# Performance work log

Hardware: AMD Instinct MI355X
Metric: run time of the kernel (lower is better)

## Reference

```python
import jax, jax.numpy as jnp
import numpy as np
import math
from jax import lax

# Fixed Poincare-ball curvature (hypll Curvature() initializes to 1.0; treated as constant here).
C_CURV = 1.0
EPS = 1e-15

def _beta(a, b):
    # Euler Beta function via lgamma (Python-level constant, computed at trace time).
    return math.exp(math.lgamma(a) + math.lgamma(b) - math.lgamma(a + b))

def logmap0(x, axis):
    # log map at the origin of the Poincare ball along `axis` (the manifold dim).
    sc = jnp.sqrt(C_CURV)
    n = jnp.sqrt(jnp.clip(jnp.sum(x * x, axis=axis, keepdims=True), EPS))
    return jnp.arctanh(jnp.clip(sc * n, 0.0, 1.0 - 1e-7)) * x / (sc * n)

def expmap0(v, axis):
    sc = jnp.sqrt(C_CURV)
    n = jnp.sqrt(jnp.clip(jnp.sum(v * v, axis=axis, keepdims=True), EPS))
    return jnp.tanh(sc * n) * v / (sc * n)

def poincare_fc(x, z, r):
    # HNN++ Poincare fully-connected layer (as in hypll): unidirectional MLR -> sinh -> ball projection.
    # x: (..., Nin) ball points, z: (Nin, Nout), r: (Nout,)
    rc = jnp.sqrt(C_CURV)
    z_norm = jnp.sqrt(jnp.clip(jnp.sum(z * z, axis=0), EPS))  # (Nout,)
    z_unit = z / z_norm
    drcr = 2.0 * rc * r
    rcx = rc * x
    cx2 = jnp.sum(rcx * rcx, axis=-1, keepdims=True)
    num = 2.0 * (rcx @ z_unit) * jnp.cosh(drcr) - (1.0 + cx2) * jnp.sinh(drcr)
    mlr = (2.0 * z_norm / rc) * jnp.arcsinh(num / jnp.clip(1.0 - cx2, EPS))
    y = jnp.sinh(rc * mlr) / rc
    return y / (1.0 + jnp.sqrt(1.0 + C_CURV * jnp.sum(y * y, axis=-1, keepdims=True)))

def hconv2d(x, z, r, k, pad):
    # Hyperbolic conv = logmap0 -> unfold -> beta-concatenation scaling -> expmap0 -> Poincare FC.
    cin = x.shape[1]
    v = logmap0(x, axis=1)  # tangent at origin, (B, C, H, W)
    patches = lax.conv_general_dilated_patches(v, (k, k), (1, 1), [(pad, pad), (pad, pad)])  # (B, C*k*k, H, W)
    scale = _beta(cin * k * k / 2.0, 0.5) / _beta(cin / 2.0, 0.5)  # HNN++ beta-concat factor
    u = expmap0(patches * scale, axis=1)
    u = jnp.transpose(u, (0, 2, 3, 1))  # (B, H, W, C*k*k)
    y = poincare_fc(u, z, r)            # (B, H, W, Cout)
    return jnp.transpose(y, (0, 3, 1, 2))

def hrelu(x, axis):
    # ReLU applied in the tangent space at the origin.
    return expmap0(jax.nn.relu(logmap0(x, axis=axis)), axis=axis)

def hmaxpool2(x):
    # 2x2 stride-2 max pool applied in the tangent space at the origin (channel man_dim=1).
    v = logmap0(x, axis=1)
    v = lax.reduce_window(v, -jnp.inf, lax.max, (1, 1, 2, 2), (1, 1, 2, 2), 'VALID')
    return expmap0(v, axis=1)

def adaptive_avg(x, out):
    # adaptive_avg_pool2d for divisible sizes == window-avg with stride H//out.
    B, C, H, W = x.shape
    f = H // out
    return x.reshape(B, C, out, f, out, f).mean(axis=(3, 5))

def setup_inputs() -> dict:
    key = jax.random.key(0)
    ks = jax.random.split(key, 14)
    B, Cin, H, W = 16, 3, 128, 128
    # input: valid Poincare-ball points via expmap0 of small tangent vectors
    x = expmap0(0.05 * jax.random.normal(ks[0], (B, Cin, H, W), jnp.float32), axis=1)
    def lin(k, fan_in, fan_out):
        return jax.random.normal(k, (fan_in, fan_out), jnp.float32) / np.float32(np.sqrt(fan_in))
    z1 = lin(ks[1], 3 * 3 * 3, 32);    b1 = 0.01 * jax.random.normal(ks[2], (32,), jnp.float32)
    z2 = lin(ks[3], 32 * 5 * 5, 64);   b2 = 0.01 * jax.random.normal(ks[4], (64,), jnp.float32)
    z3 = lin(ks[5], 64 * 7 * 7, 128);  b3 = 0.01 * jax.random.normal(ks[6], (128,), jnp.float32)
    z4 = lin(ks[7], 128 * 3 * 3, 128); b4 = 0.01 * jax.random.normal(ks[8], (128,), jnp.float32)
    zf1 = lin(ks[9], 352, 512);        bf1 = 0.01 * jax.random.normal(ks[10], (512,), jnp.float32)
    zf2 = lin(ks[11], 512, 1000);      bf2 = 0.01 * jax.random.normal(ks[12], (1000,), jnp.float32)
    return {'x': x, 'z1': z1, 'b1': b1, 'z2': z2, 'b2': b2, 'z3': z3, 'b3': b3,
            'z4': z4, 'b4': b4, 'zf1': zf1, 'bf1': bf1, 'zf2': zf2, 'bf2': bf2}

def reference(x, z1, b1, z2, b2, z3, b3, z4, b4, zf1, bf1, zf2, bf2):
    x1 = hmaxpool2(hrelu(hconv2d(x, z1, b1, 3, 1), axis=1))   # (B, 32, 64, 64)
    x2 = hmaxpool2(hrelu(hconv2d(x1, z2, b2, 5, 2), axis=1))  # (B, 64, 32, 32)
    x3 = hmaxpool2(hrelu(hconv2d(x2, z3, b3, 7, 3), axis=1))  # (B, 128, 16, 16)
    x4 = hmaxpool2(hrelu(hconv2d(x3, z4, b4, 3, 1), axis=1))  # (B, 128, 8, 8)
    t = x4.shape[2]
    cat = jnp.concatenate([adaptive_avg(x1, t), adaptive_avg(x2, t), adaptive_avg(x3, t), x4], axis=1)  # (B, 352, 8, 8)
    flat = cat.mean(axis=(2, 3))  # global avg pool -> (B, 352), treated as ball points
    h = hrelu(poincare_fc(flat, zf1, bf1), axis=-1)
    return poincare_fc(h, zf2, bf2)
```

## Files before the change

### kernel.cpp

```cpp
#include <hip/hip_runtime.h>
#include <cmath>


#define EPSF 1e-15f
#define ATANH_CAP 0.9999999f

typedef __attribute__((ext_vector_type(8))) short short8;
typedef __attribute__((ext_vector_type(4))) float f32x4;

__device__ inline unsigned rne16(float f) {
  unsigned u = __float_as_uint(f);
  return (u + 0x7FFFu + ((u >> 16) & 1u)) >> 16;
}
__device__ inline float fexp2(float x) { return __builtin_amdgcn_exp2f(x); }
__device__ inline float flog2(float x) { return __builtin_amdgcn_logf(x); }
__device__ inline float frcp(float x) { return __builtin_amdgcn_rcpf(x); }

__device__ inline float atanh_over(float n) {
  float nc = fminf(n, ATANH_CAP);
  float f = 0.34657359f * flog2((1.f + nc) * frcp(1.f - nc)) * frcp(n);
  float s = 1.f + 0.33333333f * n * n;
  return (n < 0.004f) ? s : f;
}
__device__ inline float tanh_over(float n) {
  float p2 = fexp2(2.885390082f * n);
  float f = (1.f - 2.f * frcp(p2 + 1.f)) * frcp(n);
  float s = 1.f - 0.33333333f * n * n;
  return (n < 0.004f) ? s : f;
}
__device__ inline float sinh_zasinh(float q, float twozn) {
  float aq = fabsf(q);
  float t = aq + sqrtf(fmaf(aq, aq, 1.f));
  float p = fexp2(twozn * flog2(t));
  float y = 0.5f * (p - frcp(p));
  return copysignf(y, q);
}

__global__ __launch_bounds__(256) void znorm_all_kernel(
    const float* __restrict__ z1, const float* __restrict__ z2,
    const float* __restrict__ z3, const float* __restrict__ z4,
    const float* __restrict__ zf1, const float* __restrict__ zf2,
    float* __restrict__ part) {
  const int bx = blockIdx.x;
  const float* z; int K, Nout, coff, lb;
  if (bx < 1)       { z = z1;  K = 27;   Nout = 32;   coff = 0;   lb = bx; }
  else if (bx < 2)  { z = z2;  K = 800;  Nout = 64;   coff = 32;  lb = bx - 1; }
  else if (bx < 4)  { z = z3;  K = 3136; Nout = 128;  coff = 96;  lb = bx - 2; }
  else if (bx < 6)  { z = z4;  K = 1152; Nout = 128;  coff = 224; lb = bx - 4; }
  else if (bx < 14) { z = zf1; K = 352;  Nout = 512;  coff = 352; lb = bx - 6; }
  else              { z = zf2; K = 512;  Nout = 1000; coff = 864; lb = bx - 14; }
  const int tid = threadIdx.x;
  const int col = lb * 64 + (tid & 63);
  const int kg = (blockIdx.y << 2) + (tid >> 6);
  float s = 0.f;
  if (col < Nout)
    for (int k = kg; k < K; k += 64) {
      float v = z[(size_t)k * Nout + col];
      s += v * v;
    }
  __shared__ float red[256];
  red[tid] = s;
  __syncthreads();
  if (tid < 64 && col < Nout) {
    float t = red[tid] + red[tid + 64] + red[tid + 128] + red[tid + 192];
    part[(size_t)blockIdx.y * 2048 + coff + col] = t;
  }
}
__global__ __launch_bounds__(256) void znorm_fin_kernel(
    const float* __restrict__ part, float* __restrict__ zn) {
  int c = blockIdx.x * 256 + threadIdx.x;
  float s = 0.f;
#pragma unroll
  for (int rr = 0; rr < 16; ++rr) s += part[rr * 2048 + c];
  zn[c] = sqrtf(fmaxf(s, EPSF));
}

template <int CIN, int CSH, int TAPS, int KK, int COUT>
__device__ inline void zfprep_body(int blk, const float* __restrict__ z,
                                   unsigned short* __restrict__ zh,
                                   unsigned short* __restrict__ zl) {
  constexpr int CPAD = 1 << CSH;
  constexpr int KP = TAPS * CPAD;
  constexpr int NT = COUT / 16;
  int t = blk * 256 + threadIdx.x;
  if (t >= KP * COUT) return;
  int k = t / COUT, n = t - k * COUT;
  int ks = k >> 5, lg = (k >> 3) & 3, i = k & 7;
  int nt = n >> 4, lm = n & 15;
  size_t e = ((size_t)(ks * NT + nt) * 64 + lg * 16 + lm) * 8 + i;
  int tap = k >> CSH, c = k & (CPAD - 1);
  float val = (c < CIN && tap < KK) ? z[(size_t)(c * KK + tap) * COUT + n] : 0.f;
  unsigned hi = rne16(val);
  float hif = __uint_as_float(hi << 16);
  unsigned lo = rne16(val - hif);
  zh[e] = (unsigned short)hi;
  zl[e] = (unsigned short)lo;
}
__global__ __launch_bounds__(256) void zfprep_all_kernel(
    const float* __restrict__ z1, const float* __restrict__ z2,
    const float* __restrict__ z3, const float* __restrict__ z4,
    unsigned short* __restrict__ zf1h, unsigned short* __restrict__ zf1l,
    unsigned short* __restrict__ zf2h, unsigned short* __restrict__ zf2l,
    unsigned short* __restrict__ zf3h, unsigned short* __restrict__ zf3l,
    unsigned short* __restrict__ zf4h, unsigned short* __restrict__ zf4l) {
  const int bx = blockIdx.x;
  if (bx < 12)        zfprep_body<3, 3, 12, 9, 32>(bx, z1, zf1h, zf1l);
  else if (bx < 212)  zfprep_body<32, 5, 25, 25, 64>(bx - 12, z2, zf2h, zf2l);
  else if (bx < 1780) zfprep_body<64, 6, 49, 49, 128>(bx - 212, z3, zf3h, zf3l);
  else                zfprep_body<128, 7, 9, 9, 128>(bx - 1780, z4, zf4h, zf4l);
}

__global__ __launch_bounds__(256) void logmap_s2_kernel(
    const float* __restrict__ in, float* __restrict__ out,
    float* __restrict__ s2, int C, int HW, int total) {
  int i = blockIdx.x * blockDim.x + threadIdx.x;
  if (i >= total) return;
  int b = i / HW, s = i - b * HW;
  const float* p = in + (size_t)b * C * HW + s;
  float ss = 0.f;
  for (int c = 0; c < C; ++c) { float v = p[(size_t)c * HW]; ss += v * v; }
  float n = sqrtf(fmaxf(ss, EPSF));
  float f = atanh_over(n);
  float* q = out + (size_t)b * C * HW + s;
  for (int c = 0; c < C; ++c) q[(size_t)c * HW] = f * p[(size_t)c * HW];
  s2[i] = f * f * ss;
}

__global__ __launch_bounds__(256) void wavgpool_kernel(
    const float* __restrict__ vm, const float* __restrict__ f,
    float* __restrict__ flat, int C, int HW, int flatC, int coff) {
  int c = blockIdx.x, b = blockIdx.y, tid = threadIdx.x;
  const float* p = vm + ((size_t)b * C + c) * HW;
  const float* q = f + (size_t)b * HW;
  float s = 0.f;
  for (int i = tid; i < HW; i += blockDim.x) s += p[i] * q[i];
  __shared__ float red[256];
  red[tid] = s; __syncthreads();
  for (int st = 128; st > 0; st >>= 1) {
    if (tid < st) red[tid] += red[tid + st];
    __syncthreads();
  }
  if (tid == 0) flat[(size_t)b * flatC + coff + c] = red[0] / (float)HW;
}

template <int CIN, int CSH, int TAPS, int K, int PAD, int COUT, int H, int W,
          int TH, int TW, int WM, int MREP, int WN>
__global__ __launch_bounds__(WM * WN * 64) void hconv_mfma(
    const float* __restrict__ vin, const float* __restrict__ s2map,
    const unsigned short* __restrict__ zfh,
    const unsigned short* __restrict__ zfl,
    const float* __restrict__ r, const float* __restrict__ zn,
    float* __restrict__ mout, float* __restrict__ s2out,
    float* __restrict__ fout, float scale) {
  constexpr int NTHR = WM * WN * 64;
  constexpr int CPAD = 1 << CSH;
  constexpr int KK = K * K;
  constexpr int MT = WM * MREP * 16;
  static_assert(MT == TH * TW, "tile rows mismatch");
  constexpr int NT = COUT / 16;
  constexpr int NTW = NT / WN;
  static_assert(NTW * WN == NT, "");
  constexpr int NK = TAPS * CPAD / 32;
  static_assert(NK * 32 == TAPS * CPAD, "K-step misalign");
  constexpr int SY = TH + K - 1, SX = TW + K - 1;
  constexpr int NPOS = SY * SX;
  constexpr int RWU = (CPAD >= 32) ? (CPAD + 8) : CPAD;
  constexpr int CGR = CPAD / 8;
  constexpr int TRS = MT + 4;
  constexpr int WINU = NPOS * RWU;
  constexpr int TRU = 2 * COUT * TRS;
  constexpr int SHU = (2 * WINU > TRU) ? 2 * WINU : TRU;
  constexpr int HO = H / 2, WO = W / 2;
  constexpr int PH = TH / 2, PW = TW / 2, NPP = PH * PW;
  constexpr int CG0 = NTHR / NPP;
  constexpr int CG = (CG0 < COUT) ? CG0 : COUT;
  constexpr int CPG = COUT / CG;
  static_assert(CPG * CG == COUT, "pool split");
  constexpr int SENT = 1 << 30;

  __shared__ __align__(16) unsigned short winbuf[SHU];
  __shared__ float s2w[NPOS];
  __shared__ float gA[MT], cA[MT];
  __shared__ float c1b[COUT], shb[COUT], z2b[COUT];
  __shared__ float redw[(WN > 1) ? WN * MT : 1];
  __shared__ float pacc[NTHR];
  __shared__ int stab[NK * 4];
  unsigned short* winh = winbuf;
  unsigned short* winl = winbuf + WINU;

  const int tid = threadIdx.x;
  int bid = blockIdx.x;
  constexpr int TXC = W / TW, TYC = H / TH;
  const int tx = bid % TXC; bid /= TXC;
  const int ty = bid % TYC; const int b = bid / TYC;
  const int y0 = ty * TH, x0 = tx * TW;

  if (tid < COUT) {
    float rv = r[tid];
    float znv = zn[tid];
    float ch = coshf(2.f * rv), sh = sinhf(2.f * rv);
    c1b[tid] = 2.f * ch / znv;
    shb[tid] = sh;
    z2b[tid] = 2.f * znv;
  }
  for (int i = tid; i < NK * 4; i += NTHR) {
    int ks = i >> 2, lg2 = i & 3;
    int kbase = ks * 32 + lg2 * 8;
    int tap = kbase >> CSH, c0 = kbase & (CPAD - 1);
    int v;
    if (TAPS != KK && tap >= KK) {
      v = SENT;
    } else {
      int iy = tap / K, ix = tap - (tap / K) * K;
      v = (iy * SX + ix) * RWU + c0;
    }
    stab[i] = v;
  }
  const float* vb = vin + (size_t)b * CIN * H * W;
  for (int idx = tid; idx < CGR * NPOS; idx += NTHR) {
    int pos = idx / CGR;
    int cg = idx - pos * CGR;
    int sy = pos / SX, sx = pos - sy * SX;
    int gy = y0 + sy - PAD, gx = x0 + sx - PAD;
    bool inb = (gy >= 0 && gy < H && gx >= 0 && gx < W);
    const float* gp = vb + (size_t)(cg * 8) * H * W + gy * W + gx;
    short8 hv, lv;
#pragma unroll
    for (int j = 0; j < 8; ++j) {
      float val = 0.f;
      if constexpr (CIN == CPAD) {
        if (inb) val = gp[(size_t)j * H * W];
      } else {
        if (inb && (cg * 8 + j) < CIN) val = gp[(size_t)j * H * W];
      }
      unsigned hi = rne16(val);
      float hif = __uint_as_float(hi << 16);
      unsigned lo = rne16(val - hif);
      hv[j] = (short)hi;
      lv[j] = (short)lo;
    }
    *(short8*)(winh + pos * RWU + cg * 8) = hv;
    *(short8*)(winl + pos * RWU + cg * 8) = lv;
  }
  const float* s2bp = s2map + (size_t)b * H * W;
  for (int i = tid; i < NPOS; i += NTHR) {
    int sy = i / SX, sx = i - sy * SX;
    int gy = y0 + sy - PAD, gx = x0 + sx - PAD;
    s2w[i] = (gy >= 0 && gy < H && gx >= 0 && gx < W) ? s2bp[gy * W + gx] : 0.f;
  }
  __syncthreads();

  if (tid < MT) {
    int py = tid / TW, px = tid - (tid / TW) * TW;
    float s = 0.f;
    for (int iy = 0; iy < K; ++iy)
      for (int ix = 0; ix < K; ++ix)
        s += s2w[(py + iy) * SX + (px + ix)];
    float n = sqrtf(fmaxf(scale * scale * s, EPSF));
    float th = n * tanh_over(n);
    gA[tid] = th * scale * frcp(n);
    cA[tid] = th * th;
  }
  __syncthreads();

  const int w = __builtin_amdgcn_readfirstlane(tid >> 6);
  const int wm = w % WM, wn = w / WM;
  const int lane = tid & 63, lm = lane & 15, lg = lane >> 4;
  const int nt0 = wn * NTW;

  int abase[MREP];
#pragma unroll
  for (int rep = 0; rep < MREP; ++rep) {
    int m = (wm * MREP + rep) * 16 + lm;
    int py = m / TW, px = m - (m / TW) * TW;
    abase[rep] = (py * SX + px) * RWU;
  }

  f32x4 acc[MREP][NTW];
#pragma unroll
  for (int rep = 0; rep < MREP; ++rep)
#pragma unroll
    for (int j = 0; j < NTW; ++j) acc[rep][j] = (f32x4){0.f, 0.f, 0.f, 0.f};

  const unsigned short* bph = zfh + (size_t)nt0 * 512 + lane * 8;
  const unsigned short* bpl = zfl + (size_t)nt0 * 512 + lane * 8;
  constexpr size_t BSTEP = (size_t)NT * 512;

#define LOADB(BH, BL, KS)                                             \
  do {                                                                \
    const unsigned short* ph_ = bph + (size_t)(KS)*BSTEP;             \
    const unsigned short* pl_ = bpl + (size_t)(KS)*BSTEP;             \
    _Pragma("unroll") for (int j_ = 0; j_ < NTW; ++j_) {              \
      BH[j_] = *(const uint4*)(ph_ + j_ * 512);                       \
      BL[j_] = *(const uint4*)(pl_ + j_ * 512);                       \
    }                                                                 \
  } while (0)

#define LOADA(AH, AL, KS)                                             \
  do {                                                                \
    const int so_ = stab[(KS)*4 + lg];                                \
    bool valid_ = true;                                               \
    if constexpr (TAPS != KK) valid_ = (so_ < SENT);                  \
    _Pragma("unroll") for (int r_ = 0; r_ < MREP; ++r_) {             \
      if (valid_) {                                                   \
        const int lofs_ = abase[r_] + so_;                            \
        AH[r_] = *(const short8*)(winh + lofs_);                      \
        AL[r_] = *(const short8*)(winl + lofs_);                      \
      } else {                                                        \
        AH[r_] = (short8){};                                          \
        AL[r_] = (short8){};                                          \
      }                                                               \
    }                                                                 \
  } while (0)

#define STEPK(AH, AL, BH, BL)                                         \
  do {                                                                \
    _Pragma("unroll") for (int rep_ = 0; rep_ < MREP; ++rep_) {       \
      _Pragma("unroll") for (int j_ = 0; j_ < NTW; ++j_) {            \
        short8 bhv_ = __builtin_bit_cast(short8, BH[j_]);             \
        short8 blv_ = __builtin_bit_cast(short8, BL[j_]);             \
        acc[rep_][j_] = __builtin_amdgcn_mfma_f32_16x16x32_bf16(      \
            AH[rep_], bhv_, acc[rep_][j_], 0, 0, 0);                  \
        acc[rep_][j_] = __builtin_amdgcn_mfma_f32_16x16x32_bf16(      \
            AH[rep_], blv_, acc[rep_][j_], 0, 0, 0);                  \
        acc[rep_][j_] = __builtin_amdgcn_mfma_f32_16x16x32_bf16(      \
            AL[rep_], bhv_, acc[rep_][j_], 0, 0, 0);                  \
      }                                                               \
    }                                                                 \
  } while (0)

  {
    uint4 BhA[NTW], BlA[NTW], BhB[NTW], BlB[NTW];
    short8 AhA[MREP], AlA[MREP], AhB[MREP], AlB[MREP];
    LOADB(BhA, BlA, 0);
    LOADA(AhA, AlA, 0);
    int ks = 0;
    for (;;) {
      if (ks + 1 < NK) { LOADB(BhB, BlB, ks + 1); LOADA(AhB, AlB, ks + 1); }
      STEPK(AhA, AlA, BhA, BlA);
      if (++ks == NK) break;
      if (ks + 1 < NK) { LOADB(BhA, BlA, ks + 1); LOADA(AhA, AlA, ks + 1); }
      STEPK(AhB, AlB, BhB, BlB);
      if (++ks == NK) break;
    }
  }
#undef LOADB
#undef LOADA
#undef STEPK

  float lsA[MREP][4];
#pragma unroll
  for (int rep = 0; rep < MREP; ++rep) {
    const int rbase = (wm * MREP + rep) * 16 + lg * 4;
    float ls[4] = {0.f, 0.f, 0.f, 0.f};
    float gR[4], rcpom[4], onePc[4];
#pragma unroll
    for (int reg = 0; reg < 4; ++reg) {
      float cx2 = cA[rbase + reg];
      gR[reg] = gA[rbase + reg];
      rcpom[reg] = frcp(fmaxf(1.f - cx2, EPSF));
      onePc[reg] = 1.f + cx2;
    }
#pragma unroll
    for (int j = 0; j < NTW; ++j) {
      int o = (nt0 + j) * 16 + lm;
      float c1 = c1b[o], sh = shb[o], z2 = z2b[o];
#pragma unroll
      for (int reg = 0; reg < 4; ++reg) {
        float num = c1 * (gR[reg] * acc[rep][j][reg]) - onePc[reg] * sh;
        float yv = sinh_zasinh(num * rcpom[reg], z2);
        acc[rep][j][reg] = yv;
        ls[reg] += yv * yv;
      }
    }
#pragma unroll
    for (int mask = 1; mask < 16; mask <<= 1)
#pragma unroll
      for (int reg = 0; reg < 4; ++reg)
        ls[reg] += __shfl_xor(ls[reg], mask);
#pragma unroll
    for (int reg = 0; reg < 4; ++reg) lsA[rep][reg] = ls[reg];
    if constexpr (WN > 1) {
      if (lm == 0) {
#pragma unroll
        for (int reg = 0; reg < 4; ++reg)
          redw[wn * MT + rbase + reg] = ls[reg];
      }
    }
  }
  __syncthreads();

  float* tr = (float*)winbuf;
#pragma unroll
  for (int rep = 0; rep < MREP; ++rep) {
    const int rbase = (wm * MREP + rep) * 16 + lg * 4;
    float fs[4];
#pragma unroll
    for (int reg = 0; reg < 4; ++reg) {
      float s;
      if constexpr (WN > 1) {
        s = 0.f;
#pragma unroll
        for (int k2 = 0; k2 < WN; ++k2) s += redw[k2 * MT + rbase + reg];
      } else {
        s = lsA[rep][reg];
      }
      float inv = frcp(1.f + sqrtf(1.f + s));
      float ny = sqrtf(fmaxf(s * inv * inv, EPSF));
      fs[reg] = atanh_over(ny) * inv;
    }
#pragma unroll
    for (int j = 0; j < NTW; ++j) {
      int o = (nt0 + j) * 16 + lm;
#pragma unroll
      for (int reg = 0; reg < 4; ++reg)
        tr[o * TRS + rbase + reg] = fs[reg] * fmaxf(acc[rep][j][reg], 0.f);
    }
  }
  __syncthreads();

  const int y0p = y0 >> 1, x0p = x0 >> 1;
  if (tid < NPP * CG) {
    int cg = tid / NPP, p = tid - cg * NPP;
    int ppy = p / PW, ppx = p - ppy * PW;
    const float* base = tr + (ppy * 2) * TW + ppx * 2;
    float ss = 0.f;
#pragma unroll
    for (int j = 0; j < CPG; ++j) {
      int c = cg * CPG + j;
      const float* rp = base + c * TRS;
      float mv = fmaxf(fmaxf(rp[0], rp[1]), fmaxf(rp[TW], rp[TW + 1]));
      mout[((size_t)(b * COUT + c) * HO + y0p + ppy) * WO + x0p + ppx] = mv;
      ss += mv * mv;
    }
    pacc[cg * NPP + p] = ss;
  }
  __syncthreads();
  if (tid < NPP) {
    float ss = 0.f;
    for (int k2 = 0; k2 < CG; ++k2) ss += pacc[k2 * NPP + tid];
    int ppy = tid / PW, ppx = tid - (tid / PW) * PW;
    size_t pix = ((size_t)b * HO + y0p + ppy) * WO + x0p + ppx;
    s2out[pix] = ss;
    float n = sqrtf(fmaxf(ss, EPSF));
    fout[pix] = tanh_over(n);
  }
}

template <int NIN, int NOUT, bool POS>
__global__ __launch_bounds__(256) void pfc_y_kernel(
    const float* __restrict__ x, const float* __restrict__ z,
    const float* __restrict__ r, const float* __restrict__ zn,
    float* __restrict__ ybuf, float* __restrict__ part,
    float* __restrict__ partpos) {
  constexpr int KCH = NIN / 4;
  const int b = blockIdx.y, tid = threadIdx.x;
  const int nt = gridDim.x;
  const int o = blockIdx.x * 64 + (tid & 63);
  const int kg = tid >> 6;
  __shared__ float xs[NIN];
  __shared__ float red[256];
  for (int i = tid; i < NIN; i += 256) xs[i] = x[(size_t)b * NIN + i];
  __syncthreads();
  float s = 0.f;
  for (int i = tid; i < NIN; i += 256) { float v = xs[i]; s += v * v; }
  red[tid] = s;
  __syncthreads();
  for (int st = 128; st > 0; st >>= 1) {
    if (tid < st) red[tid] += red[tid + st];
    __syncthreads();
  }
  const float cx2 = red[0];
  __syncthreads();
  float d = 0.f;
  if (o < NOUT) {
    const float* zp = z + (size_t)(kg * KCH) * NOUT + o;
    const float* xp = xs + kg * KCH;
    for (int k = 0; k < KCH; ++k) d = fmaf(xp[k], zp[(size_t)k * NOUT], d);
  }
  red[tid] = d;
  __syncthreads();
  if (tid < 64) {
    float dot = red[tid] + red[tid + 64] + red[tid + 128] + red[tid + 192];
    float y = 0.f;
    if (o < NOUT) {
      float znv = zn[o], rv = r[o];
      float onemc = fmaxf(1.f - cx2, EPSF);
      float num = 2.f * (dot / znv) * coshf(2.f * rv) - (1.f + cx2) * sinhf(2.f * rv);
      y = sinh_zasinh(num * frcp(onemc), 2.f * znv);
      ybuf[(size_t)b * NOUT + o] = y;
    }
    float ls = y * y;
    float lp = POS ? (fmaxf(y, 0.f) * fmaxf(y, 0.f)) : 0.f;
#pragma unroll
    for (int mask = 1; mask < 64; mask <<= 1) {
      ls += __shfl_xor(ls, mask);
      if (POS) lp += __shfl_xor(lp, mask);
    }
    if (tid == 0) {
      part[(size_t)b * nt + blockIdx.x] = ls;
      if (POS) partpos[(size_t)b * nt + blockIdx.x] = lp;
    }
  }
}

template <int NOUT, int NT>
__global__ __launch_bounds__(256) void pfc_fin_hrelu_kernel(
    const float* __restrict__ ybuf, const float* __restrict__ part,
    const float* __restrict__ partpos, float* __restrict__ h) {
  const int b = blockIdx.x, tid = threadIdx.x;
  float s = 0.f, sp = 0.f;
#pragma unroll
  for (int t = 0; t < NT; ++t) {
    s += part[(size_t)b * NT + t];
    sp += partpos[(size_t)b * NT + t];
  }
  float inv = frcp(1.f + sqrtf(1.f + s));
  float ny = sqrtf(fmaxf(s, EPSF)) * inv;
  float fl = atanh_over(ny) * inv;
  float nw = fl * sqrtf(fmaxf(sp, EPSF));
  float gg = tanh_over(nw);
  float cmb = gg * fl;
  for (int o = tid; o < NOUT; o += 256)
    h[(size_t)b * NOUT + o] = cmb * fmaxf(ybuf[(size_t)b * NOUT + o], 0.f);
}

template <int NOUT, int NT>
__global__ __launch_bounds__(256) void pfc_fin_kernel(
    const float* __restrict__ ybuf, const float* __restrict__ part,
    float* __restrict__ out) {
  const int b = blockIdx.x, tid = threadIdx.x;
  float s = 0.f;
#pragma unroll
  for (int t = 0; t < NT; ++t) s += part[(size_t)b * NT + t];
  float inv = frcp(1.f + sqrtf(1.f + s));
  for (int o = tid; o < NOUT; o += 256)
    out[(size_t)b * NOUT + o] = ybuf[(size_t)b * NOUT + o] * inv;
}

static inline double beta_fn(double a, double b) {
  return std::exp(std::lgamma(a) + std::lgamma(b) - std::lgamma(a + b));
}

extern "C" void kernel_launch(void* const* d_in, const int* in_sizes, int n_in,
                              void* d_out, int out_size, void* d_ws, size_t ws_size,
                              hipStream_t stream) {
  const float* x   = (const float*)d_in[0];
  const float* z1  = (const float*)d_in[1];
  const float* b1  = (const float*)d_in[2];
  const float* z2  = (const float*)d_in[3];
  const float* b2  = (const float*)d_in[4];
  const float* z3  = (const float*)d_in[5];
  const float* b3  = (const float*)d_in[6];
  const float* z4  = (const float*)d_in[7];
  const float* b4  = (const float*)d_in[8];
  const float* zf1 = (const float*)d_in[9];
  const float* bf1 = (const float*)d_in[10];
  const float* zf2 = (const float*)d_in[11];
  const float* bf2 = (const float*)d_in[12];
  float* outp = (float*)d_out;

  float* ws    = (float*)d_ws;
  float* zn    = ws;
  float* flat  = ws + 2048;
  float* h1r   = ws + 7680;
  float* h1    = ws + 15872;
  float* vm0   = ws + 24576;
  float* mA    = vm0 + 786432;
  float* mB    = mA + 2097152;
  float* s2a   = mB + 1048576;
  float* s2b   = s2a + 262144;
  float* fA    = s2b + 65536;
  float* fB    = fA + 65536;
  float* part  = fB + 16384;
  unsigned short* zfu = (unsigned short*)(part + 32768);
  unsigned short* zf1h = zfu;
  unsigned short* zf1l = zfu + 3072;
  unsigned short* zf2h = zfu + 6144;
  unsigned short* zf2l = zfu + 57344;
  unsigned short* zf3h = zfu + 108544;
  unsigned short* zf3l = zfu + 509952;
  unsigned short* zf4h = zfu + 911360;
  unsigned short* zf4l = zfu + 1058816;
  float* yb2  = part + 32768 + 603136;
  float* hp1  = yb2 + 16000;
  float* hpp1 = hp1 + 128;
  float* hp2  = hpp1 + 128;

  const float s1  = (float)(beta_fn(27.0 / 2.0, 0.5) / beta_fn(3.0 / 2.0, 0.5));
  const float s2c = (float)(beta_fn(800.0 / 2.0, 0.5) / beta_fn(32.0 / 2.0, 0.5));
  const float s3  = (float)(beta_fn(3136.0 / 2.0, 0.5) / beta_fn(64.0 / 2.0, 0.5));
  const float s4  = (float)(beta_fn(1152.0 / 2.0, 0.5) / beta_fn(128.0 / 2.0, 0.5));

  auto g1 = [](int n) { return dim3((n + 255) / 256); };

  znorm_all_kernel<<<dim3(30, 16), 256, 0, stream>>>(z1, z2, z3, z4, zf1, zf2, part);
  znorm_fin_kernel<<<8, 256, 0, stream>>>(part, zn);
  zfprep_all_kernel<<<2356, 256, 0, stream>>>(z1, z2, z3, z4, zf1h, zf1l,
                                              zf2h, zf2l, zf3h, zf3l, zf4h, zf4l);

  logmap_s2_kernel<<<g1(262144), 256, 0, stream>>>(x, vm0, s2a, 3, 16384, 262144);
  hconv_mfma<3, 3, 12, 3, 1, 32, 128, 128, 8, 8, 4, 1, 1>
      <<<4096, 256, 0, stream>>>(vm0, s2a, zf1h, zf1l, b1, zn + 0, mA, s2b, fA, s1);
  wavgpool_kernel<<<dim3(32, 16), 256, 0, stream>>>(mA, fA, flat, 32, 4096, 352, 0);

  hconv_mfma<32, 5, 25, 5, 2, 64, 64, 64, 8, 8, 2, 2, 2>
      <<<1024, 256, 0, stream>>>(mA, s2b, zf2h, zf2l, b2, zn + 32, mB, s2a, fB, s2c);
  wavgpool_kernel<<<dim3(64, 16), 256, 0, stream>>>(mB, fB, flat, 64, 1024, 352, 32);

  hconv_mfma<64, 6, 49, 7, 3, 128, 32, 32, 4, 8, 1, 2, 8>
      <<<512, 512, 0, stream>>>(mB, s2a, zf3h, zf3l, b3, zn + 96, mA, s2b, fA, s3);
  wavgpool_kernel<<<dim3(128, 16), 256, 0, stream>>>(mA, fA, flat, 128, 256, 352, 96);

  hconv_mfma<128, 7, 9, 3, 1, 128, 16, 16, 2, 8, 1, 1, 8>
      <<<256, 512, 0, stream>>>(mA, s2b, zf4h, zf4l, b4, zn + 224, mB, s2a, fB, s4);
  wavgpool_kernel<<<dim3(128, 16), 256, 0, stream>>>(mB, fB, flat, 128, 64, 352, 224);

  pfc_y_kernel<352, 512, true><<<dim3(8, 16), 256, 0, stream>>>(
      flat, zf1, bf1, zn + 352, h1r, hp1, hpp1);
  pfc_fin_hrelu_kernel<512, 8><<<16, 256, 0, stream>>>(h1r, hp1, hpp1, h1);
  pfc_y_kernel<512, 1000, false><<<dim3(16, 16), 256, 0, stream>>>(
      h1, zf2, bf2, zn + 864, yb2, hp2, nullptr);
  pfc_fin_kernel<1000, 16><<<16, 256, 0, stream>>>(yb2, hp2, outp);

  (void)in_sizes; (void)n_in; (void)out_size; (void)ws_size;
}
```

Measured before the change: 184.5 us.

## Fuse logmap into first conv, batch avgpools, fold hrelu into FC2

The standalone logmap kernel is removed and its work moves into the first conv's tile-loading stage, which computes the norm, atanh factor and s2 inline from raw input. The four weighted avg-pool launches become one kernel over all 352 channels, with each layer output kept in its own buffer. The hrelu finalisation kernel is folded into the second FC kernel's input load. The third conv's WN changes from 8 to 4, halving its block to 256 threads. Together these cut several launches and a full intermediate write/read. In exchange, first-layer blocks recompute logmap on halo pixels, and the smaller conv3 blocks may change occupancy.

```diff
diff --git a/kernel.cpp b/kernel.cpp
--- a/kernel.cpp
+++ b/kernel.cpp
@@ -110,41 +110,33 @@
   else                zfprep_body<128, 7, 9, 9, 128>(bx - 1780, z4, zf4h, zf4l);
 }
 
-__global__ __launch_bounds__(256) void logmap_s2_kernel(
-    const float* __restrict__ in, float* __restrict__ out,
-    float* __restrict__ s2, int C, int HW, int total) {
-  int i = blockIdx.x * blockDim.x + threadIdx.x;
-  if (i >= total) return;
-  int b = i / HW, s = i - b * HW;
-  const float* p = in + (size_t)b * C * HW + s;
-  float ss = 0.f;
-  for (int c = 0; c < C; ++c) { float v = p[(size_t)c * HW]; ss += v * v; }
-  float n = sqrtf(fmaxf(ss, EPSF));
-  float f = atanh_over(n);
-  float* q = out + (size_t)b * C * HW + s;
-  for (int c = 0; c < C; ++c) q[(size_t)c * HW] = f * p[(size_t)c * HW];
-  s2[i] = f * f * ss;
-}
-
-__global__ __launch_bounds__(256) void wavgpool_kernel(
-    const float* __restrict__ vm, const float* __restrict__ f,
-    float* __restrict__ flat, int C, int HW, int flatC, int coff) {
-  int c = blockIdx.x, b = blockIdx.y, tid = threadIdx.x;
-  const float* p = vm + ((size_t)b * C + c) * HW;
+__global__ __launch_bounds__(256) void wavgpool_all_kernel(
+    const float* __restrict__ m1, const float* __restrict__ m2,
+    const float* __restrict__ m3, const float* __restrict__ m4,
+    const float* __restrict__ f1, const float* __restrict__ f2,
+    const float* __restrict__ f3, const float* __restrict__ f4,
+    float* __restrict__ flat) {
+  const int c = blockIdx.x, b = blockIdx.y, tid = threadIdx.x;
+  const float* m; const float* f; int HW, C, cl;
+  if (c < 32)       { m = m1; f = f1; HW = 4096; C = 32;  cl = c; }
+  else if (c < 96)  { m = m2; f = f2; HW = 1024; C = 64;  cl = c - 32; }
+  else if (c < 224) { m = m3; f = f3; HW = 256;  C = 128; cl = c - 96; }
+  else              { m = m4; f = f4; HW = 64;   C = 128; cl = c - 224; }
+  const float* p = m + ((size_t)b * C + cl) * HW;
   const float* q = f + (size_t)b * HW;
   float s = 0.f;
-  for (int i = tid; i < HW; i += blockDim.x) s += p[i] * q[i];
+  for (int i = tid; i < HW; i += 256) s += p[i] * q[i];
   __shared__ float red[256];
   red[tid] = s; __syncthreads();
   for (int st = 128; st > 0; st >>= 1) {
     if (tid < st) red[tid] += red[tid + st];
     __syncthreads();
   }
-  if (tid == 0) flat[(size_t)b * flatC + coff + c] = red[0] / (float)HW;
+  if (tid == 0) flat[(size_t)b * 352 + c] = red[0] / (float)HW;
 }
 
 template <int CIN, int CSH, int TAPS, int K, int PAD, int COUT, int H, int W,
-          int TH, int TW, int WM, int MREP, int WN>
+          int TH, int TW, int WM, int MREP, int WN, bool FLOG>
 __global__ __launch_bounds__(WM * WN * 64) void hconv_mfma(
     const float* __restrict__ vin, const float* __restrict__ s2map,
     const unsigned short* __restrict__ zfh,
@@ -217,36 +209,68 @@
     stab[i] = v;
   }
   const float* vb = vin + (size_t)b * CIN * H * W;
-  for (int idx = tid; idx < CGR * NPOS; idx += NTHR) {
-    int pos = idx / CGR;
-    int cg = idx - pos * CGR;
-    int sy = pos / SX, sx = pos - sy * SX;
-    int gy = y0 + sy - PAD, gx = x0 + sx - PAD;
-    bool inb = (gy >= 0 && gy < H && gx >= 0 && gx < W);
-    const float* gp = vb + (size_t)(cg * 8) * H * W + gy * W + gx;
-    short8 hv, lv;
-#pragma unroll
-    for (int j = 0; j < 8; ++j) {
-      float val = 0.f;
-      if constexpr (CIN == CPAD) {
-        if (inb) val = gp[(size_t)j * H * W];
-      } else {
-        if (inb && (cg * 8 + j) < CIN) val = gp[(size_t)j * H * W];
+  if constexpr (FLOG) {
+    static_assert(CIN == 3 && CPAD == 8, "FLOG expects CIN=3");
+    for (int pos = tid; pos < NPOS; pos += NTHR) {
+      int sy = pos / SX, sx = pos - sy * SX;
+      int gy = y0 + sy - PAD, gx = x0 + sx - PAD;
+      bool inb = (gy >= 0 && gy < H && gx >= 0 && gx < W);
+      float v0 = 0.f, v1 = 0.f, v2 = 0.f;
+      if (inb) {
+        const float* gp = vb + gy * W + gx;
+        v0 = gp[0];
+        v1 = gp[(size_t)H * W];
+        v2 = gp[(size_t)2 * H * W];
       }
-      unsigned hi = rne16(val);
-      float hif = __uint_as_float(hi << 16);
-      unsigned lo = rne16(val - hif);
-      hv[j] = (short)hi;
-      lv[j] = (short)lo;
-    }
-    *(short8*)(winh + pos * RWU + cg * 8) = hv;
-    *(short8*)(winl + pos * RWU + cg * 8) = lv;
-  }
-  const float* s2bp = s2map + (size_t)b * H * W;
-  for (int i = tid; i < NPOS; i += NTHR) {
-    int sy = i / SX, sx = i - sy * SX;
-    int gy = y0 + sy - PAD, gx = x0 + sx - PAD;
-    s2w[i] = (gy >= 0 && gy < H && gx >= 0 && gx < W) ? s2bp[gy * W + gx] : 0.f;
+      float ssr = v0 * v0 + v1 * v1 + v2 * v2;
+      float n = sqrtf(fmaxf(ssr, EPSF));
+      float f = atanh_over(n);
+      s2w[pos] = f * f * ssr;
+      float vals[8] = {f * v0, f * v1, f * v2, 0.f, 0.f, 0.f, 0.f, 0.f};
+      short8 hv, lv;
+#pragma unroll
+      for (int j = 0; j < 8; ++j) {
+        unsigned hi = rne16(vals[j]);
+        float hif = __uint_as_float(hi << 16);
+        unsigned lo = rne16(vals[j] - hif);
+        hv[j] = (short)hi;
+        lv[j] = (short)lo;
+      }
+      *(short8*)(winh + pos * RWU) = hv;
+      *(short8*)(winl + pos * RWU) = lv;
+    }
+  } else {
+    for (int idx = tid; idx < CGR * NPOS; idx += NTHR) {
+      int pos = idx / CGR;
+      int cg = idx - pos * CGR;
+      int sy = pos / SX, sx = pos - sy * SX;
+      int gy = y0 + sy - PAD, gx = x0 + sx - PAD;
+      bool inb = (gy >= 0 && gy < H && gx >= 0 && gx < W);
+      const float* gp = vb + (size_t)(cg * 8) * H * W + gy * W + gx;
+      short8 hv, lv;
+#pragma unroll
+      for (int j = 0; j < 8; ++j) {
+        float val = 0.f;
+        if constexpr (CIN == CPAD) {
+          if (inb) val = gp[(size_t)j * H * W];
+        } else {
+          if (inb && (cg * 8 + j) < CIN) val = gp[(size_t)j * H * W];
+        }
+        unsigned hi = rne16(val);
+        float hif = __uint_as_float(hi << 16);
+        unsigned lo = rne16(val - hif);
+        hv[j] = (short)hi;
+        lv[j] = (short)lo;
+      }
+      *(short8*)(winh + pos * RWU + cg * 8) = hv;
+      *(short8*)(winl + pos * RWU + cg * 8) = lv;
+    }
+    const float* s2bp = s2map + (size_t)b * H * W;
+    for (int i = tid; i < NPOS; i += NTHR) {
+      int sy = i / SX, sx = i - sy * SX;
+      int gy = y0 + sy - PAD, gx = x0 + sx - PAD;
+      s2w[i] = (gy >= 0 && gy < H && gx >= 0 && gx < W) ? s2bp[gy * W + gx] : 0.f;
+    }
   }
   __syncthreads();
 
@@ -447,12 +471,13 @@
   }
 }
 
-template <int NIN, int NOUT, bool POS>
+template <int NIN, int NOUT, bool POS, bool FUSEH, int NTP>
 __global__ __launch_bounds__(256) void pfc_y_kernel(
     const float* __restrict__ x, const float* __restrict__ z,
     const float* __restrict__ r, const float* __restrict__ zn,
     float* __restrict__ ybuf, float* __restrict__ part,
-    float* __restrict__ partpos) {
+    float* __restrict__ partpos, const float* __restrict__ pin,
+    const float* __restrict__ pinpos) {
   constexpr int KCH = NIN / 4;
   const int b = blockIdx.y, tid = threadIdx.x;
   const int nt = gridDim.x;
@@ -460,7 +485,24 @@
   const int kg = tid >> 6;
   __shared__ float xs[NIN];
   __shared__ float red[256];
-  for (int i = tid; i < NIN; i += 256) xs[i] = x[(size_t)b * NIN + i];
+  float cmb = 1.f;
+  if constexpr (FUSEH) {
+    float s = 0.f, sp = 0.f;
+#pragma unroll
+    for (int t = 0; t < NTP; ++t) {
+      s += pin[(size_t)b * NTP + t];
+      sp += pinpos[(size_t)b * NTP + t];
+    }
+    float inv = frcp(1.f + sqrtf(1.f + s));
+    float ny = sqrtf(fmaxf(s, EPSF)) * inv;
+    float fl = atanh_over(ny) * inv;
+    float nw = fl * sqrtf(fmaxf(sp, EPSF));
+    cmb = tanh_over(nw) * fl;
+  }
+  for (int i = tid; i < NIN; i += 256) {
+    float v = x[(size_t)b * NIN + i];
+    xs[i] = FUSEH ? cmb * fmaxf(v, 0.f) : v;
+  }
   __syncthreads();
   float s = 0.f;
   for (int i = tid; i < NIN; i += 256) { float v = xs[i]; s += v * v; }
@@ -502,27 +544,6 @@
       if (POS) partpos[(size_t)b * nt + blockIdx.x] = lp;
     }
   }
-}
-
-template <int NOUT, int NT>
-__global__ __launch_bounds__(256) void pfc_fin_hrelu_kernel(
-    const float* __restrict__ ybuf, const float* __restrict__ part,
-    const float* __restrict__ partpos, float* __restrict__ h) {
-  const int b = blockIdx.x, tid = threadIdx.x;
-  float s = 0.f, sp = 0.f;
-#pragma unroll
-  for (int t = 0; t < NT; ++t) {
-    s += part[(size_t)b * NT + t];
-    sp += partpos[(size_t)b * NT + t];
-  }
-  float inv = frcp(1.f + sqrtf(1.f + s));
-  float ny = sqrtf(fmaxf(s, EPSF)) * inv;
-  float fl = atanh_over(ny) * inv;
-  float nw = fl * sqrtf(fmaxf(sp, EPSF));
-  float gg = tanh_over(nw);
-  float cmb = gg * fl;
-  for (int o = tid; o < NOUT; o += 256)
-    h[(size_t)b * NOUT + o] = cmb * fmaxf(ybuf[(size_t)b * NOUT + o], 0.f);
 }
 
 template <int NOUT, int NT>
@@ -563,17 +584,25 @@
   float* ws    = (float*)d_ws;
   float* zn    = ws;
   float* flat  = ws + 2048;
-  float* h1r   = ws + 7680;
-  float* h1    = ws + 15872;
-  float* vm0   = ws + 24576;
-  float* mA    = vm0 + 786432;
-  float* mB    = mA + 2097152;
-  float* s2a   = mB + 1048576;
-  float* s2b   = s2a + 262144;
-  float* fA    = s2b + 65536;
-  float* fB    = fA + 65536;
-  float* part  = fB + 16384;
-  unsigned short* zfu = (unsigned short*)(part + 32768);
+  float* yb1   = ws + 7680;
+  float* yb2   = ws + 15872;
+  float* hp1   = ws + 31872;
+  float* hpp1  = ws + 32000;
+  float* hp2   = ws + 32128;
+  float* part  = ws + 32768;
+  float* m1    = ws + 65536;
+  float* m2    = m1 + 2097152;
+  float* m3    = m2 + 1048576;
+  float* m4    = m3 + 524288;
+  float* s1b   = m4 + 131072;
+  float* s2bf  = s1b + 65536;
+  float* s3b   = s2bf + 16384;
+  float* s4b   = s3b + 4096;
+  float* f1    = s4b + 1024;
+  float* f2    = f1 + 65536;
+  float* f3    = f2 + 16384;
+  float* f4    = f3 + 4096;
+  unsigned short* zfu = (unsigned short*)(f4 + 1024);
   unsigned short* zf1h = zfu;
   unsigned short* zf1l = zfu + 3072;
   unsigned short* zf2h = zfu + 6144;
@@ -582,45 +611,36 @@
   unsigned short* zf3l = zfu + 509952;
   unsigned short* zf4h = zfu + 911360;
   unsigned short* zf4l = zfu + 1058816;
-  float* yb2  = part + 32768 + 603136;
-  float* hp1  = yb2 + 16000;
-  float* hpp1 = hp1 + 128;
-  float* hp2  = hpp1 + 128;
 
   const float s1  = (float)(beta_fn(27.0 / 2.0, 0.5) / beta_fn(3.0 / 2.0, 0.5));
   const float s2c = (float)(beta_fn(800.0 / 2.0, 0.5) / beta_fn(32.0 / 2.0, 0.5));
   const float s3  = (float)(beta_fn(3136.0 / 2.0, 0.5) / beta_fn(64.0 / 2.0, 0.5));
   const float s4  = (float)(beta_fn(1152.0 / 2.0, 0.5) / beta_fn(128.0 / 2.0, 0.5));
 
-  auto g1 = [](int n) { return dim3((n + 255) / 256); };
-
   znorm_all_kernel<<<dim3(30, 16), 256, 0, stream>>>(z1, z2, z3, z4, zf1, zf2, part);
   znorm_fin_kernel<<<8, 256, 0, stream>>>(part, zn);
   zfprep_all_kernel<<<2356, 256, 0, stream>>>(z1, z2, z3, z4, zf1h, zf1l,
                                               zf2h, zf2l, zf3h, zf3l, zf4h, zf4l);
 
-  logmap_s2_kernel<<<g1(262144), 256, 0, stream>>>(x, vm0, s2a, 3, 16384, 262144);
-  hconv_mfma<3, 3, 12, 3, 1, 32, 128, 128, 8, 8, 4, 1, 1>
-      <<<4096, 256, 0, stream>>>(vm0, s2a, zf1h, zf1l, b1, zn + 0, mA, s2b, fA, s1);
-  wavgpool_kernel<<<dim3(32, 16), 256, 0, stream>>>(mA, fA, flat, 32, 4096, 352, 0);
-
-  hconv_mfma<32, 5, 25, 5, 2, 64, 64, 64, 8, 8, 2, 2, 2>
-      <<<1024, 256, 0, stream>>>(mA, s2b, zf2h, zf2l, b2, zn + 32, mB, s2a, fB, s2c);
-  wavgpool_kernel<<<dim3(64, 16), 256, 0, stream>>>(mB, fB, flat, 64, 1024, 352, 32);
-
-  hconv_mfma<64, 6, 49, 7, 3, 128, 32, 32, 4, 8, 1, 2, 8>
-      <<<512, 512, 0, stream>>>(mB, s2a, zf3h, zf3l, b3, zn + 96, mA, s2b, fA, s3);
-  wavgpool_kernel<<<dim3(128, 16), 256, 0, stream>>>(mA, fA, flat, 128, 256, 352, 96);
-
-  hconv_mfma<128, 7, 9, 3, 1, 128, 16, 16, 2, 8, 1, 1, 8>
-      <<<256, 512, 0, stream>>>(mA, s2b, zf4h, zf4l, b4, zn + 224, mB, s2a, fB, s4);
-  wavgpool_kernel<<<dim3(128, 16), 256, 0, stream>>>(mB, fB, flat, 128, 64, 352, 224);
-
-  pfc_y_kernel<352, 512, true><<<dim3(8, 16), 256, 0, stream>>>(
-      flat, zf1, bf1, zn + 352, h1r, hp1, hpp1);
-  pfc_fin_hrelu_kernel<512, 8><<<16, 256, 0, stream>>>(h1r, hp1, hpp1, h1);
-  pfc_y_kernel<512, 1000, false><<<dim3(16, 16), 256, 0, stream>>>(
-      h1, zf2, bf2, zn + 864, yb2, hp2, nullptr);
+  hconv_mfma<3, 3, 12, 3, 1, 32, 128, 128, 8, 8, 4, 1, 1, true>
+      <<<4096, 256, 0, stream>>>(x, nullptr, zf1h, zf1l, b1, zn + 0, m1, s1b, f1, s1);
+
+  hconv_mfma<32, 5, 25, 5, 2, 64, 64, 64, 8, 8, 2, 2, 2, false>
+      <<<1024, 256, 0, stream>>>(m1, s1b, zf2h, zf2l, b2, zn + 32, m2, s2bf, f2, s2c);
+
+  hconv_mfma<64, 6, 49, 7, 3, 128, 32, 32, 4, 8, 1, 2, 4, false>
+      <<<512, 256, 0, stream>>>(m2, s2bf, zf3h, zf3l, b3, zn + 96, m3, s3b, f3, s3);
+
+  hconv_mfma<128, 7, 9, 3, 1, 128, 16, 16, 2, 8, 1, 1, 8, false>
+      <<<256, 512, 0, stream>>>(m3, s3b, zf4h, zf4l, b4, zn + 224, m4, s4b, f4, s4);
+
+  wavgpool_all_kernel<<<dim3(352, 16), 256, 0, stream>>>(
+      m1, m2, m3, m4, f1, f2, f3, f4, flat);
+
+  pfc_y_kernel<352, 512, true, false, 0><<<dim3(8, 16), 256, 0, stream>>>(
+      flat, zf1, bf1, zn + 352, yb1, hp1, hpp1, nullptr, nullptr);
+  pfc_y_kernel<512, 1000, false, true, 8><<<dim3(16, 16), 256, 0, stream>>>(
+      yb1, zf2, bf2, zn + 864, yb2, hp2, nullptr, hp1, hpp1);
   pfc_fin_kernel<1000, 16><<<16, 256, 0, stream>>>(yb2, hp2, outp);
 
   (void)in_sizes; (void)n_in; (void)out_size; (void)ws_size;
```

Result: faster. 170.9 us (-7.4%).
